# Performance work log

Hardware: AMD Instinct MI355X
Metric: run time of the kernel (lower is better)

The kernel has to match this reference:

```python
import jax, jax.numpy as jnp
import numpy as np

B, IN_DIM, OUT_DIM = 4096, 2048, 2048
EMA_M = 0.95
LN_EPS = 1e-5


def setup_inputs() -> dict:
    key = jax.random.key(0)
    ks = jax.random.split(key, 8)
    x = jax.random.normal(ks[0], (B, IN_DIM), dtype=jnp.float32)
    # W_slow is orthogonal-init in torch (gain 0.5); scaled gaussian is a fine stand-in for math testing
    W_slow = jax.random.normal(ks[1], (OUT_DIM, IN_DIM), dtype=jnp.float32) * (0.5 / np.sqrt(IN_DIM))
    # buffers start at zero in torch; use small nonzero values so the medium/fast GEMMs are exercised
    W_medium = jax.random.normal(ks[2], (OUT_DIM, IN_DIM), dtype=jnp.float32) * 0.01
    W_fast = jax.random.normal(ks[3], (OUT_DIM, IN_DIM), dtype=jnp.float32) * 0.01
    ln_gamma = jnp.ones((OUT_DIM,), jnp.float32) + 0.1 * jax.random.normal(ks[4], (OUT_DIM,), dtype=jnp.float32)
    ln_beta = 0.1 * jax.random.normal(ks[5], (OUT_DIM,), dtype=jnp.float32)
    pc_w1 = jax.random.normal(ks[6], (8, 3), dtype=jnp.float32) * 0.5
    pc_b1 = jnp.zeros((8,), jnp.float32)
    pc_w2 = jax.random.normal(ks[7], (1, 8), dtype=jnp.float32) * 0.5
    pc_b2 = jnp.full((1,), -1.5, jnp.float32)  # torch fills last Linear bias with -1.5
    ema_mean = jnp.zeros((1,), jnp.float32)
    ema_std = jnp.ones((1,), jnp.float32)
    return {"x": x, "W_slow": W_slow, "W_medium": W_medium, "W_fast": W_fast,
            "ln_gamma": ln_gamma, "ln_beta": ln_beta,
            "pc_w1": pc_w1, "pc_b1": pc_b1, "pc_w2": pc_w2, "pc_b2": pc_b2,
            "ema_mean": ema_mean, "ema_std": ema_std}


def reference(x, W_slow, W_medium, W_fast, ln_gamma, ln_beta,
              pc_w1, pc_b1, pc_w2, pc_b2, ema_mean, ema_std):
    xc = jnp.clip(x, -5.0, 5.0)
    slow_out = jnp.clip(xc @ W_slow.T, -10.0, 10.0)
    pre_act = jnp.clip(slow_out + xc @ W_medium.T + xc @ W_fast.T, -10.0, 10.0)  # [B, OUT]

    batch_mean = pre_act.mean(axis=1, keepdims=True)                      # [B,1]
    batch_std = jnp.maximum(pre_act.std(axis=1, keepdims=True), 1e-6)     # [B,1], ddof=0

    # EMA buffer update (no-grad in torch); clamps applied after update
    new_mean = jnp.clip(EMA_M * ema_mean + (1.0 - EMA_M) * batch_mean.mean(), -0.5, 0.5)
    new_std = jnp.clip(EMA_M * ema_std + (1.0 - EMA_M) * batch_std.mean(), 0.1, 1.5)
    homeostasis = new_std / (jnp.abs(new_mean) + 1e-6)                    # [1]

    stats = jnp.concatenate([batch_mean, batch_std,
                             jnp.broadcast_to(homeostasis[None, :], (batch_mean.shape[0], 1))], axis=1)  # [B,3]
    h = jax.nn.gelu(stats @ pc_w1.T + pc_b1, approximate=False)           # torch GELU is exact erf
    learned_plasticity = jax.nn.sigmoid(h @ pc_w2.T + pc_b2)[:, 0]        # [B] (does not affect `out`)
    _ = learned_plasticity  # kept for fidelity with original compute graph

    # LayerNorm over last dim, eps=1e-5
    mu = pre_act.mean(axis=-1, keepdims=True)
    var = pre_act.var(axis=-1, keepdims=True)
    normed = (pre_act - mu) * jax.lax.rsqrt(var + LN_EPS) * ln_gamma + ln_beta
    out = 5.0 * jnp.tanh(normed / 5.0)
    return out
```

## Files before the change

### kernel.cpp

```cpp
#include <hip/hip_runtime.h>
#include <hip/hip_bf16.h>

#define BDIM    4096
#define IN_DIM  2048
#define OUT_DIM 2048

typedef __attribute__((ext_vector_type(4))) float  floatx4;
typedef __attribute__((ext_vector_type(8))) short  bf16x8;

__device__ __forceinline__ unsigned short f2bf(float f) {
    union { float f; unsigned u; } v; v.f = f;
    unsigned r = v.u + 0x7FFFu + ((v.u >> 16) & 1u);
    return (unsigned short)(r >> 16);
}

__device__ __forceinline__ void async16(const unsigned short* g, unsigned short* l) {
    __builtin_amdgcn_global_load_lds(
        (const __attribute__((address_space(1))) unsigned int*)g,
        (__attribute__((address_space(3))) unsigned int*)l,
        16, 0, 0);
}

__global__ __launch_bounds__(256) void prep(const float* __restrict__ x,
                                            const float* __restrict__ Ws,
                                            const float* __restrict__ Wm,
                                            const float* __restrict__ Wf,
                                            unsigned short* __restrict__ xc,
                                            unsigned short* __restrict__ bsum) {
    int b = blockIdx.x;
    if (b < 8192) {
        int i = b * 256 + threadIdx.x;
        float4 v = ((const float4*)x)[i];
        ushort4 o;
        o.x = f2bf(fminf(fmaxf(v.x, -5.f), 5.f));
        o.y = f2bf(fminf(fmaxf(v.y, -5.f), 5.f));
        o.z = f2bf(fminf(fmaxf(v.z, -5.f), 5.f));
        o.w = f2bf(fminf(fmaxf(v.w, -5.f), 5.f));
        ((ushort4*)xc)[i] = o;
    } else {
        int i = (b - 8192) * 256 + threadIdx.x;
        float4 s = ((const float4*)Ws)[i];
        float4 m = ((const float4*)Wm)[i];
        float4 f = ((const float4*)Wf)[i];
        ushort4 o;
        o.x = f2bf(s.x + m.x + f.x);
        o.y = f2bf(s.y + m.y + f.y);
        o.z = f2bf(s.z + m.z + f.z);
        o.w = f2bf(s.w + m.w + f.w);
        ((ushort4*)bsum)[i] = o;
    }
}

#define TILE 128
#define BK   32

__global__ __launch_bounds__(256) void gemm_bt(const unsigned short* __restrict__ A,
                                               const unsigned short* __restrict__ B,
                                               float* __restrict__ C) {
    constexpr int N = OUT_DIM, K = IN_DIM;
    __shared__ __align__(16) unsigned short As[TILE * BK];
    __shared__ __align__(16) unsigned short Bs[TILE * BK];

    const int tid  = threadIdx.x;
    const int lane = tid & 63;
    const int wave = tid >> 6;
    const int wm   = (wave >> 1) * 64;
    const int wn   = (wave & 1) * 64;
    const int rowBlock = blockIdx.y * TILE;
    const int colBlock = blockIdx.x * TILE;

    const int sRow = tid >> 2;
    const int sCol = (tid & 3) * 8;
    const unsigned short* aBase = A + (size_t)(rowBlock + sRow) * K + sCol;
    const unsigned short* bBase = B + (size_t)(colBlock + sRow) * K + sCol;
    unsigned short* AsDst = As + tid * 8;
    unsigned short* BsDst = Bs + tid * 8;

    floatx4 acc[4][4] = {};

    const int fragRow = lane & 15;
    const int kOff    = (lane >> 4) * 8;

    for (int k0 = 0; k0 < K; k0 += BK) {
        async16(aBase + k0,                   AsDst);
        async16(aBase + (size_t)64 * K + k0,  AsDst + 64 * BK);
        async16(bBase + k0,                   BsDst);
        async16(bBase + (size_t)64 * K + k0,  BsDst + 64 * BK);
        __syncthreads();

        bf16x8 af[4], bfr[4];
#pragma unroll
        for (int i = 0; i < 4; i++) {
            af[i]  = *(const bf16x8*)(As + (wm + i * 16 + fragRow) * BK + kOff);
            bfr[i] = *(const bf16x8*)(Bs + (wn + i * 16 + fragRow) * BK + kOff);
        }
#pragma unroll
        for (int i = 0; i < 4; i++)
#pragma unroll
            for (int j = 0; j < 4; j++)
                acc[i][j] = __builtin_amdgcn_mfma_f32_16x16x32_bf16(af[i], bfr[j], acc[i][j], 0, 0, 0);
        __syncthreads();
    }

    const int cCol = colBlock + wn + (lane & 15);
    const int cRow = rowBlock + wm + (lane >> 4) * 4;
#pragma unroll
    for (int i = 0; i < 4; i++) {
#pragma unroll
        for (int j = 0; j < 4; j++) {
            const int col = cCol + j * 16;
            const int rb  = cRow + i * 16;
#pragma unroll
            for (int r = 0; r < 4; r++)
                C[(size_t)(rb + r) * N + col] = acc[i][j][r];
        }
    }
}

__global__ __launch_bounds__(256) void ln_kernel(const float* __restrict__ C,
                                                 const float* __restrict__ gamma,
                                                 const float* __restrict__ beta,
                                                 float* __restrict__ out) {
    const int row = blockIdx.x;
    const int tid = threadIdx.x;
    __shared__ __align__(16) float pre[OUT_DIM];
    __shared__ float wsum[4], wsq[4];

    const float4* Cr = (const float4*)(C + (size_t)row * OUT_DIM);

    float sum = 0.f, sq = 0.f;
#pragma unroll
    for (int it = 0; it < OUT_DIM / 4 / 256; it++) {
        int i = tid + it * 256;
        float4 c = Cr[i];
        float4 p;
        p.x = fminf(fmaxf(c.x, -10.f), 10.f);
        p.y = fminf(fmaxf(c.y, -10.f), 10.f);
        p.z = fminf(fmaxf(c.z, -10.f), 10.f);
        p.w = fminf(fmaxf(c.w, -10.f), 10.f);
        *(float4*)(pre + i * 4) = p;
        sum += p.x + p.y + p.z + p.w;
        sq  += p.x * p.x + p.y * p.y + p.z * p.z + p.w * p.w;
    }
#pragma unroll
    for (int off = 32; off > 0; off >>= 1) {
        sum += __shfl_down(sum, off);
        sq  += __shfl_down(sq,  off);
    }
    if ((tid & 63) == 0) { wsum[tid >> 6] = sum; wsq[tid >> 6] = sq; }
    __syncthreads();
    const float tsum = wsum[0] + wsum[1] + wsum[2] + wsum[3];
    const float tsq  = wsq[0]  + wsq[1]  + wsq[2]  + wsq[3];
    const float mu   = tsum * (1.0f / OUT_DIM);
    const float var  = tsq * (1.0f / OUT_DIM) - mu * mu;
    const float inv  = rsqrtf(var + 1e-5f);

#pragma unroll
    for (int it = 0; it < OUT_DIM / 4 / 256; it++) {
        int i = tid + it * 256;
        float4 p = *(const float4*)(pre + i * 4);
        float4 g = *(const float4*)(gamma + i * 4);
        float4 b = *(const float4*)(beta + i * 4);
        float4 o;
        float zx = (p.x - mu) * inv * g.x + b.x;
        float zy = (p.y - mu) * inv * g.y + b.y;
        float zz = (p.z - mu) * inv * g.z + b.z;
        float zw = (p.w - mu) * inv * g.w + b.w;
        o.x = 5.f * (1.f - 2.f / (__expf(0.4f * zx) + 1.f));
        o.y = 5.f * (1.f - 2.f / (__expf(0.4f * zy) + 1.f));
        o.z = 5.f * (1.f - 2.f / (__expf(0.4f * zz) + 1.f));
        o.w = 5.f * (1.f - 2.f / (__expf(0.4f * zw) + 1.f));
        *(float4*)(out + (size_t)row * OUT_DIM + i * 4) = o;
    }
}

extern "C" void kernel_launch(void* const* d_in, const int* in_sizes, int n_in,
                              void* d_out, int out_size, void* d_ws, size_t ws_size,
                              hipStream_t stream) {
    const float* x     = (const float*)d_in[0];
    const float* Ws    = (const float*)d_in[1];
    const float* Wm    = (const float*)d_in[2];
    const float* Wf    = (const float*)d_in[3];
    const float* gamma = (const float*)d_in[4];
    const float* beta  = (const float*)d_in[5];
    float* out = (float*)d_out;

    char* ws = (char*)d_ws;
    unsigned short* xc   = (unsigned short*)ws;
    unsigned short* bsum = (unsigned short*)(ws + (size_t)16 * 1024 * 1024);
    float*          Cbuf = (float*)(ws + (size_t)24 * 1024 * 1024);

    prep<<<12288, 256, 0, stream>>>(x, Ws, Wm, Wf, xc, bsum);
    dim3 g(OUT_DIM / TILE, BDIM / TILE);
    gemm_bt<<<g, 256, 0, stream>>>(xc, bsum, Cbuf);
    ln_kernel<<<BDIM, 256, 0, stream>>>(Cbuf, gamma, beta, out);
}
```

Before: 196.4 us.

## Split GEMM along K, widen K tile with XOR-swizzled LDS, sum partials in LN

The GEMM grid gains a z dimension of 2, and each block computes half of the K range into its own fp32 partial buffer. The LayerNorm kernel adds the two partials before clipping and keeps the values in registers instead of shared memory. The K tile doubles to 64, which halves the number of barrier pairs per block. An XOR swizzle on the LDS segment layout is meant to avoid bank conflicts on fragment reads. In exchange, an extra 32MB partial buffer is written and read back, and the workspace must be large enough to hold both partials.

Measured after the change: 204.2 us. 4.0% more time.

```diff
diff --git a/kernel.cpp b/kernel.cpp
--- a/kernel.cpp
+++ b/kernel.cpp
@@ -51,12 +51,14 @@
     }
 }
 
-#define TILE 128
-#define BK   32
+#define TILE   128
+#define BK     64
+#define KSPLIT 2
+#define KHALF  (IN_DIM / KSPLIT)
 
 __global__ __launch_bounds__(256) void gemm_bt(const unsigned short* __restrict__ A,
                                                const unsigned short* __restrict__ B,
-                                               float* __restrict__ C) {
+                                               float* __restrict__ Cpart) {
     constexpr int N = OUT_DIM, K = IN_DIM;
     __shared__ __align__(16) unsigned short As[TILE * BK];
     __shared__ __align__(16) unsigned short Bs[TILE * BK];
@@ -68,37 +70,46 @@
     const int wn   = (wave & 1) * 64;
     const int rowBlock = blockIdx.y * TILE;
     const int colBlock = blockIdx.x * TILE;
-
-    const int sRow = tid >> 2;
-    const int sCol = (tid & 3) * 8;
-    const unsigned short* aBase = A + (size_t)(rowBlock + sRow) * K + sCol;
-    const unsigned short* bBase = B + (size_t)(colBlock + sRow) * K + sCol;
+    const int kBase    = blockIdx.z * KHALF;
+    float* C = Cpart + (size_t)blockIdx.z * BDIM * OUT_DIM;
+
+    const int sRow = tid >> 3;
+    const int sSeg = (tid & 7) ^ (sRow & 7);
+    const unsigned short* aSrc = A + (size_t)(rowBlock + sRow) * K + kBase + sSeg * 8;
+    const unsigned short* bSrc = B + (size_t)(colBlock + sRow) * K + kBase + sSeg * 8;
     unsigned short* AsDst = As + tid * 8;
     unsigned short* BsDst = Bs + tid * 8;
 
     floatx4 acc[4][4] = {};
 
     const int fragRow = lane & 15;
-    const int kOff    = (lane >> 4) * 8;
-
-    for (int k0 = 0; k0 < K; k0 += BK) {
-        async16(aBase + k0,                   AsDst);
-        async16(aBase + (size_t)64 * K + k0,  AsDst + 64 * BK);
-        async16(bBase + k0,                   BsDst);
-        async16(bBase + (size_t)64 * K + k0,  BsDst + 64 * BK);
+    const int quad    = lane >> 4;
+    const int l7      = lane & 7;
+
+    for (int k0 = 0; k0 < KHALF; k0 += BK) {
+#pragma unroll
+        for (int r = 0; r < 4; r++)
+            async16(aSrc + k0 + (size_t)(r * 32) * K, AsDst + r * 32 * BK);
+#pragma unroll
+        for (int r = 0; r < 4; r++)
+            async16(bSrc + k0 + (size_t)(r * 32) * K, BsDst + r * 32 * BK);
         __syncthreads();
 
-        bf16x8 af[4], bfr[4];
-#pragma unroll
-        for (int i = 0; i < 4; i++) {
-            af[i]  = *(const bf16x8*)(As + (wm + i * 16 + fragRow) * BK + kOff);
-            bfr[i] = *(const bf16x8*)(Bs + (wn + i * 16 + fragRow) * BK + kOff);
+#pragma unroll
+        for (int kk = 0; kk < 2; kk++) {
+            const int xs = ((quad + kk * 4) ^ l7) << 3;
+            bf16x8 af[4], bfr[4];
+#pragma unroll
+            for (int i = 0; i < 4; i++) {
+                af[i]  = *(const bf16x8*)(As + (wm + i * 16 + fragRow) * BK + xs);
+                bfr[i] = *(const bf16x8*)(Bs + (wn + i * 16 + fragRow) * BK + xs);
+            }
+#pragma unroll
+            for (int i = 0; i < 4; i++)
+#pragma unroll
+                for (int j = 0; j < 4; j++)
+                    acc[i][j] = __builtin_amdgcn_mfma_f32_16x16x32_bf16(af[i], bfr[j], acc[i][j], 0, 0, 0);
         }
-#pragma unroll
-        for (int i = 0; i < 4; i++)
-#pragma unroll
-            for (int j = 0; j < 4; j++)
-                acc[i][j] = __builtin_amdgcn_mfma_f32_16x16x32_bf16(af[i], bfr[j], acc[i][j], 0, 0, 0);
         __syncthreads();
     }
 
@@ -117,30 +128,32 @@
     }
 }
 
-__global__ __launch_bounds__(256) void ln_kernel(const float* __restrict__ C,
+__global__ __launch_bounds__(256) void ln_kernel(const float* __restrict__ Cpart,
                                                  const float* __restrict__ gamma,
                                                  const float* __restrict__ beta,
                                                  float* __restrict__ out) {
     const int row = blockIdx.x;
     const int tid = threadIdx.x;
-    __shared__ __align__(16) float pre[OUT_DIM];
     __shared__ float wsum[4], wsq[4];
 
-    const float4* Cr = (const float4*)(C + (size_t)row * OUT_DIM);
-
+    const float4* Ca = (const float4*)(Cpart + (size_t)row * OUT_DIM);
+    const float4* Cb = (const float4*)(Cpart + (size_t)BDIM * OUT_DIM + (size_t)row * OUT_DIM);
+
+    float4 p[2];
     float sum = 0.f, sq = 0.f;
 #pragma unroll
-    for (int it = 0; it < OUT_DIM / 4 / 256; it++) {
+    for (int it = 0; it < 2; it++) {
         int i = tid + it * 256;
-        float4 c = Cr[i];
-        float4 p;
-        p.x = fminf(fmaxf(c.x, -10.f), 10.f);
-        p.y = fminf(fmaxf(c.y, -10.f), 10.f);
-        p.z = fminf(fmaxf(c.z, -10.f), 10.f);
-        p.w = fminf(fmaxf(c.w, -10.f), 10.f);
-        *(float4*)(pre + i * 4) = p;
-        sum += p.x + p.y + p.z + p.w;
-        sq  += p.x * p.x + p.y * p.y + p.z * p.z + p.w * p.w;
+        float4 a = Ca[i];
+        float4 b = Cb[i];
+        float4 q;
+        q.x = fminf(fmaxf(a.x + b.x, -10.f), 10.f);
+        q.y = fminf(fmaxf(a.y + b.y, -10.f), 10.f);
+        q.z = fminf(fmaxf(a.z + b.z, -10.f), 10.f);
+        q.w = fminf(fmaxf(a.w + b.w, -10.f), 10.f);
+        p[it] = q;
+        sum += q.x + q.y + q.z + q.w;
+        sq  += q.x * q.x + q.y * q.y + q.z * q.z + q.w * q.w;
     }
 #pragma unroll
     for (int off = 32; off > 0; off >>= 1) {
@@ -156,16 +169,16 @@
     const float inv  = rsqrtf(var + 1e-5f);
 
 #pragma unroll
-    for (int it = 0; it < OUT_DIM / 4 / 256; it++) {
+    for (int it = 0; it < 2; it++) {
         int i = tid + it * 256;
-        float4 p = *(const float4*)(pre + i * 4);
+        float4 q = p[it];
         float4 g = *(const float4*)(gamma + i * 4);
         float4 b = *(const float4*)(beta + i * 4);
         float4 o;
-        float zx = (p.x - mu) * inv * g.x + b.x;
-        float zy = (p.y - mu) * inv * g.y + b.y;
-        float zz = (p.z - mu) * inv * g.z + b.z;
-        float zw = (p.w - mu) * inv * g.w + b.w;
+        float zx = (q.x - mu) * inv * g.x + b.x;
+        float zy = (q.y - mu) * inv * g.y + b.y;
+        float zz = (q.z - mu) * inv * g.z + b.z;
+        float zw = (q.w - mu) * inv * g.w + b.w;
         o.x = 5.f * (1.f - 2.f / (__expf(0.4f * zx) + 1.f));
         o.y = 5.f * (1.f - 2.f / (__expf(0.4f * zy) + 1.f));
         o.z = 5.f * (1.f - 2.f / (__expf(0.4f * zz) + 1.f));
@@ -191,7 +204,7 @@
     float*          Cbuf = (float*)(ws + (size_t)24 * 1024 * 1024);
 
     prep<<<12288, 256, 0, stream>>>(x, Ws, Wm, Wf, xc, bsum);
-    dim3 g(OUT_DIM / TILE, BDIM / TILE);
+    dim3 g(OUT_DIM / TILE, BDIM / TILE, KSPLIT);
     gemm_bt<<<g, 256, 0, stream>>>(xc, bsum, Cbuf);
     ln_kernel<<<BDIM, 256, 0, stream>>>(Cbuf, gamma, beta, out);
 }
```
